# Performance work log

Hardware: AMD Instinct MI355X
Metric: run time of the kernel (lower is better)

## Reference

```python
import jax, jax.numpy as jnp
import numpy as np

N, E, R = 10000, 320000, 32
IN, H, OUT, REL_IN = 256, 256, 256, 768
GAMMA = 10.0


def _seg_softmax(logits, seg, n):
    # numerically stable softmax over edges grouped by target node
    m = jax.ops.segment_max(logits, seg, num_segments=n)
    e = jnp.exp(logits - m[seg])
    s = jax.ops.segment_sum(e, seg, num_segments=n)
    return e / (s[seg] + 1e-16)


def _rgat_layer(x, src, dst, etype, W, q, k, n):
    # per-relation linear transform of all nodes: [N, R, H]
    xt = jnp.einsum('ni,rio->nro', x, W)
    xj = xt[src, etype]          # [E, H] transformed source feats
    xi = xt[dst, etype]          # [E, H] transformed target feats
    logits = jax.nn.leaky_relu((xi * q[etype]).sum(-1) + (xj * k[etype]).sum(-1), 0.2)
    a = _seg_softmax(logits, dst, n)            # [E]
    return jax.ops.segment_sum(a[:, None] * xj, dst, num_segments=n)  # [N, H]


def setup_inputs() -> dict:
    key = jax.random.key(0)
    ks = jax.random.split(key, 16)
    s = 0.05
    return {
        'x': jax.random.normal(ks[0], (N, IN), jnp.float32),
        'edge_index': jax.random.randint(ks[1], (2, E), 0, N, jnp.int32),
        'edge_type': jax.random.randint(ks[2], (E,), 0, R, jnp.int32),
        'W1': jax.random.normal(ks[3], (R, IN, H), jnp.float32) * s,
        'q1': jax.random.normal(ks[4], (R, H), jnp.float32) * s,
        'k1': jax.random.normal(ks[5], (R, H), jnp.float32) * s,
        'W2': jax.random.normal(ks[6], (R, H, H), jnp.float32) * s,
        'q2': jax.random.normal(ks[7], (R, H), jnp.float32) * s,
        'k2': jax.random.normal(ks[8], (R, H), jnp.float32) * s,
        'lin_w': jax.random.normal(ks[9], (H, OUT), jnp.float32) * s,
        'lin_b': jnp.zeros((OUT,), jnp.float32),
        'rel_bert': jax.random.normal(ks[10], (R, REL_IN), jnp.float32),
        'rel_lin_w': jax.random.normal(ks[11], (REL_IN, H), jnp.float32) * s,
        'rel_lin_b': jnp.zeros((H,), jnp.float32),
    }


def reference(x, edge_index, edge_type, W1, q1, k1, W2, q2, k2,
              lin_w, lin_b, rel_bert, rel_lin_w, rel_lin_b):
    src, dst = edge_index[0], edge_index[1]
    h = jax.nn.relu(_rgat_layer(x, src, dst, edge_type, W1, q1, k1, N))
    h = jax.nn.relu(_rgat_layer(h, src, dst, edge_type, W2, q2, k2, N))
    h = h @ lin_w + lin_b                                   # [N, OUT]
    # relation embeddings (dropout omitted: eval-mode determinism)
    rel = jax.nn.relu(rel_bert @ rel_lin_w + rel_lin_b)     # [R, H]
    # TransE scoring per edge
    diff = h[src] + rel[edge_type] - h[dst]                 # [E, OUT]
    score = GAMMA - jnp.abs(diff).sum(-1)                   # [E]
    return score
```

## Files before the change

### kernel.cpp

```cpp
#include <hip/hip_runtime.h>
#include <hip/hip_bf16.h>
#include <stdint.h>

#define R_ 32
#define H_ 256
#define GAMMA_ 10.0f

typedef __attribute__((ext_vector_type(4))) float f32x4;
typedef __attribute__((ext_vector_type(8))) short bf16x8;

__device__ __forceinline__ unsigned short f2b(float f){
  union { float f; unsigned u; } v; v.f = f;
  unsigned r = v.u + 0x7FFFu + ((v.u >> 16) & 1u);
  return (unsigned short)(r >> 16);
}
__device__ __forceinline__ float b2f(unsigned short h){
  union { unsigned u; float f; } v; v.u = ((unsigned)h) << 16; return v.f;
}

__global__ __launch_bounds__(256) void prep_kernel(
    const float* __restrict__ x, unsigned short* __restrict__ xb, int n4,
    const float* __restrict__ W1, unsigned short* __restrict__ Wt1,
    const float* __restrict__ W2, unsigned short* __restrict__ Wt2,
    const float* __restrict__ lin_w, unsigned short* __restrict__ linT,
    const float* __restrict__ q1, const float* __restrict__ k1, float* __restrict__ wqkT1,
    const float* __restrict__ q2, const float* __restrict__ k2, float* __restrict__ wqkT2,
    const float* __restrict__ rb, const float* __restrict__ rw,
    const float* __restrict__ rbias, unsigned short* __restrict__ relb,
    const int* __restrict__ dst, const int* __restrict__ et, int* __restrict__ cnt2, int E,
    int nb0, int nb_tw, int nb_lin, int nb_wqk, int nb_rel, int nb_hist){
  __shared__ float tile[32][33];
  const int bx = blockIdx.x, t = threadIdx.x;
  const int b0 = nb0, b1 = b0 + nb_tw, b2 = b1 + nb_tw, b3 = b2 + nb_lin;
  const int b4 = b3 + nb_wqk, b5 = b4 + nb_wqk, b6 = b5 + nb_rel;

  if (bx < b0){
    int i = bx * 256 + t;
    if (i < n4){
      float4 v = ((const float4*)x)[i];
      ushort4 o; o.x=f2b(v.x); o.y=f2b(v.y); o.z=f2b(v.z); o.w=f2b(v.w);
      ((ushort4*)xb)[i] = o;
    }
    return;
  }
  if (bx < b3){
    const float* W; unsigned short* Wt; int local;
    if (bx < b1){ W = W1; Wt = Wt1; local = bx - b0; }
    else if (bx < b2){ W = W2; Wt = Wt2; local = bx - b1; }
    else { W = lin_w; Wt = linT; local = bx - b2; }
    int i0 = (local & 7) * 32, o0 = ((local >> 3) & 7) * 32, r = local >> 6;
    int tx = t & 31, ty = t >> 5;
    const float* Wr = W + (size_t)r * 65536;
    for (int rr = ty; rr < 32; rr += 8)
      tile[rr][tx] = Wr[(size_t)(i0 + rr) * 256 + o0 + tx];
    __syncthreads();
    unsigned short* outr = Wt + (size_t)r * 65536;
    for (int rr = ty; rr < 32; rr += 8)
      outr[(size_t)(o0 + rr) * 256 + i0 + tx] = f2b(tile[tx][rr]);
    return;
  }
  if (bx < b5){
    bool first = bx < b4;
    int local = bx - (first ? b3 : b4);
    int w = t >> 6, lane = t & 63;
    int p = local * 4 + w;
    int i = p & 255, r = p >> 8;
    const float* W  = first ? W1 : W2;
    const float* qv = first ? q1 : q2;
    const float* kv = first ? k1 : k2;
    const float* row = W + ((size_t)r * 256 + i) * 256;
    float sq = 0.f, sk = 0.f;
    #pragma unroll
    for (int q4 = 0; q4 < 4; ++q4){
      int o = lane + q4 * 64;
      float wv = row[o];
      sq += wv * qv[r * 256 + o];
      sk += wv * kv[r * 256 + o];
    }
    #pragma unroll
    for (int o = 32; o; o >>= 1){ sq += __shfl_xor(sq, o); sk += __shfl_xor(sk, o); }
    if (!lane){
      float* wq = first ? wqkT1 : wqkT2;
      wq[i * 64 + r] = sq; wq[i * 64 + 32 + r] = sk;
    }
    return;
  }
  if (bx < b6){
    int r = bx - b5, h = t;
    float acc = rbias[h];
    const float* br = rb + (size_t)r * 768;
    for (int i = 0; i < 768; ++i) acc += br[i] * rw[(size_t)i * 256 + h];
    relb[r * 256 + h] = f2b(fmaxf(acc, 0.f));
    return;
  }
  {
    int e = (bx - b6) * 256 + t;
    if (e < E){
      int d = dst[e];
      atomicAdd(&cnt2[(d >> 5) * 1024 + (d & 31) * 32 + et[e]], 1);
    }
  }
}

__global__ void totred_kernel(const int* __restrict__ cnt2, int* __restrict__ tot){
  __shared__ int red[256];
  int blk = blockIdx.x, t = threadIdx.x;
  int s = 0;
  #pragma unroll
  for (int q = 0; q < 4; ++q) s += cnt2[blk * 1024 + q * 256 + t];
  red[t] = s; __syncthreads();
  for (int o = 128; o; o >>= 1){ if (t < o) red[t] += red[t + o]; __syncthreads(); }
  if (!t) tot[blk] = red[0];
}
__global__ void scan_kernel(const int* __restrict__ deg, int* __restrict__ off, int n){
  __shared__ int carry;
  __shared__ int buf[1024];
  if (threadIdx.x == 0) carry = 0;
  __syncthreads();
  for (int base = 0; base < n; base += 1024){
    int i = base + threadIdx.x;
    int v = (i < n) ? deg[i] : 0;
    buf[threadIdx.x] = v; __syncthreads();
    for (int o = 1; o < 1024; o <<= 1){
      int t = (threadIdx.x >= o) ? buf[threadIdx.x - o] : 0;
      __syncthreads();
      buf[threadIdx.x] += t;
      __syncthreads();
    }
    if (i < n) off[i] = carry + buf[threadIdx.x] - v;
    __syncthreads();
    if (threadIdx.x == 1023) carry += buf[1023];
    __syncthreads();
  }
  if (threadIdx.x == 0) off[n] = carry;
}
__global__ __launch_bounds__(256) void ps2scan_kernel(const int* __restrict__ cnt2, const int* __restrict__ base,
                                                      int* __restrict__ ps2, int nblk, int nbins){
  __shared__ int sb[1024];
  int blk = blockIdx.x, t = threadIdx.x;
  int orig[4];
  #pragma unroll
  for (int q = 0; q < 4; ++q){ int i = q * 256 + t; orig[q] = cnt2[blk * 1024 + i]; sb[i] = orig[q]; }
  __syncthreads();
  for (int o = 1; o < 1024; o <<= 1){
    int v[4];
    #pragma unroll
    for (int q = 0; q < 4; ++q){ int i = q * 256 + t; v[q] = (i >= o) ? sb[i - o] : 0; }
    __syncthreads();
    #pragma unroll
    for (int q = 0; q < 4; ++q){ int i = q * 256 + t; sb[i] += v[q]; }
    __syncthreads();
  }
  int b = base[blk];
  #pragma unroll
  for (int q = 0; q < 4; ++q){ int i = q * 256 + t; ps2[blk * 1024 + i] = b + sb[i] - orig[q]; }
  if (blk == 0 && t == 0) ps2[nbins] = base[nblk];
}
__global__ void scatter2_kernel(const int* __restrict__ src, const int* __restrict__ dst,
                                const int* __restrict__ et, const int* __restrict__ ps2,
                                int* __restrict__ cur2, int* __restrict__ es_src,
                                int* __restrict__ es_et, int E){
  int e = blockIdx.x * 256 + threadIdx.x;
  if (e >= E) return;
  int d = dst[e], r = et[e];
  int key = (d >> 5) * 1024 + (d & 31) * 32 + r;
  int pos = ps2[key] + atomicAdd(&cur2[key], 1);
  es_src[pos] = src[e];
  es_et[pos]  = r;
}

template<int MODE>
__global__ __launch_bounds__(256) void gemmq_kernel(
    const unsigned short* __restrict__ A, const unsigned short* __restrict__ Bt,
    unsigned short* __restrict__ C, const float* __restrict__ bias, int M, int g_gemm,
    const float* __restrict__ wqkT, float* __restrict__ qdot, float* __restrict__ kdot){
  __shared__ unsigned short As[2][128 * 32];
  __shared__ unsigned short Bs[2][128 * 32];
  const int tid = threadIdx.x, lane = tid & 63, wid = tid >> 6;
  const int bx = blockIdx.x;

  if (MODE == 0 && bx >= g_gemm){
    int node = (bx - g_gemm) * 4 + wid;
    if (node >= M) return;
    float* xr = ((float*)As) + wid * 256;
    ushort4 v = ((const ushort4*)(A + (size_t)node * 256))[lane];
    xr[lane * 4 + 0] = b2f(v.x);
    xr[lane * 4 + 1] = b2f(v.y);
    xr[lane * 4 + 2] = b2f(v.z);
    xr[lane * 4 + 3] = b2f(v.w);
    float acc = 0.f;
    #pragma unroll 8
    for (int kk = 0; kk < 256; ++kk)
      acc = fmaf(xr[kk], wqkT[kk * 64 + lane], acc);
    if (lane < 32) qdot[node * 32 + lane] = acc;
    else           kdot[node * 32 + lane - 32] = acc;
    return;
  }

  const int x = (MODE == 0) ? (bx & 63) : (bx & 1);
  const int y = (MODE == 0) ? (bx >> 6) : (bx >> 1);
  const int r = (MODE == 0) ? (x >> 1) : 0;
  const int nbase = (x & 1) * 128;
  const int mbase = y * 128;
  const int wm = (wid >> 1) * 64, wn = (wid & 1) * 64;
  const int lg = lane >> 4, lr = lane & 15;
  const unsigned short* Brel = Bt + (size_t)r * 65536;

  f32x4 acc[4][4];
  #pragma unroll
  for (int i = 0; i < 4; ++i)
    #pragma unroll
    for (int j = 0; j < 4; ++j) acc[i][j] = (f32x4)0.0f;

  auto stage = [&](int buf, int kt){
    #pragma unroll
    for (int q = 0; q < 2; ++q){
      int ci = q * 256 + tid;
      int row = ci >> 2, p = ci & 3;
      int gch = p ^ ((row >> 1) & 3);
      int grow = mbase + row; if (grow >= M) grow = M - 1;
      const unsigned short* ga = A + (size_t)grow * 256 + kt * 32 + gch * 8;
      __builtin_amdgcn_global_load_lds((const __attribute__((address_space(1))) void*)ga,
          (__attribute__((address_space(3))) void*)(As[buf] + (size_t)ci * 8), 16, 0, 0);
      const unsigned short* gb = Brel + (size_t)(nbase + row) * 256 + kt * 32 + gch * 8;
      __builtin_amdgcn_global_load_lds((const __attribute__((address_space(1))) void*)gb,
          (__attribute__((address_space(3))) void*)(Bs[buf] + (size_t)ci * 8), 16, 0, 0);
    }
  };

  stage(0, 0);
  __syncthreads();

  for (int kt = 0; kt < 8; ++kt){
    const int cur = kt & 1;
    if (kt < 7) stage(cur ^ 1, kt + 1);
    bf16x8 af[4], bg[4];
    #pragma unroll
    for (int mi = 0; mi < 4; ++mi){
      int row = wm + mi * 16 + lr;
      int sl = lg ^ ((row >> 1) & 3);
      af[mi] = *(const bf16x8*)&As[cur][row * 32 + sl * 8];
    }
    #pragma unroll
    for (int ni = 0; ni < 4; ++ni){
      int row = wn + ni * 16 + lr;
      int sl = lg ^ ((row >> 1) & 3);
      bg[ni] = *(const bf16x8*)&Bs[cur][row * 32 + sl * 8];
    }
    #pragma unroll
    for (int mi = 0; mi < 4; ++mi)
      #pragma unroll
      for (int ni = 0; ni < 4; ++ni)
        acc[mi][ni] = __builtin_amdgcn_mfma_f32_16x16x32_bf16(af[mi], bg[ni], acc[mi][ni], 0, 0, 0);
    __syncthreads();
  }

  #pragma unroll
  for (int mi = 0; mi < 4; ++mi){
    #pragma unroll
    for (int j = 0; j < 4; ++j){
      int rowm = mbase + wm + mi * 16 + lg * 4 + j;
      if (rowm >= M) continue;
      #pragma unroll
      for (int ni = 0; ni < 4; ++ni){
        int col = nbase + wn + ni * 16 + lr;
        float v = acc[mi][ni][j];
        if (MODE == 0) C[((size_t)r * M + rowm) * H_ + col] = f2b(v);
        else           C[(size_t)rowm * H_ + col] = f2b(v + bias[col]);
      }
    }
  }
}

__global__ void attn_agg_kernel(const unsigned short* __restrict__ xt, const float* __restrict__ qdot,
                                const float* __restrict__ kdot, const int* __restrict__ ps2,
                                const int* __restrict__ es_src, const int* __restrict__ es_et,
                                float* __restrict__ a, unsigned short* __restrict__ hout, int n){
  int w = threadIdx.x >> 6, lane = threadIdx.x & 63;
  int node = blockIdx.x * 4 + w;
  if (node >= n) return;
  int kb = (node >> 5) * 1024 + (node & 31) * 32;
  int s = 0, e = 0;
  float qd = 0.f;
  if (lane < 32){
    s = ps2[kb + lane]; e = ps2[kb + lane + 1];
    qd = qdot[node * 32 + lane];
  }
  float m = -1e30f;
  for (int j = s; j < e; ++j){
    float z = qd + kdot[es_src[j] * 32 + lane];
    z = (z > 0.f) ? z : 0.2f * z;
    a[j] = z;
    m = fmaxf(m, z);
  }
  #pragma unroll
  for (int o = 32; o; o >>= 1) m = fmaxf(m, __shfl_xor(m, o));
  float sum = 0.f;
  for (int j = s; j < e; ++j){
    float ez = __expf(a[j] - m);
    a[j] = ez; sum += ez;
  }
  #pragma unroll
  for (int o = 32; o; o >>= 1) sum += __shfl_xor(sum, o);
  float inv = 1.0f / (sum + 1e-16f);
  int s0 = ps2[kb], s1 = ps2[kb + 32];
  float a0 = 0.f, a1 = 0.f, a2 = 0.f, a3 = 0.f;
  int j = s0;
  for (; j + 4 <= s1; j += 4){
    int sc0 = es_src[j],   et0 = es_et[j];
    int sc1 = es_src[j+1], et1 = es_et[j+1];
    int sc2 = es_src[j+2], et2 = es_et[j+2];
    int sc3 = es_src[j+3], et3 = es_et[j+3];
    float w0 = a[j], w1 = a[j+1], w2 = a[j+2], w3 = a[j+3];
    ushort4 v0 = ((const ushort4*)(xt + ((size_t)et0 * n + sc0) * 256))[lane];
    ushort4 v1 = ((const ushort4*)(xt + ((size_t)et1 * n + sc1) * 256))[lane];
    ushort4 v2 = ((const ushort4*)(xt + ((size_t)et2 * n + sc2) * 256))[lane];
    ushort4 v3 = ((const ushort4*)(xt + ((size_t)et3 * n + sc3) * 256))[lane];
    a0 += w0*b2f(v0.x) + w1*b2f(v1.x) + w2*b2f(v2.x) + w3*b2f(v3.x);
    a1 += w0*b2f(v0.y) + w1*b2f(v1.y) + w2*b2f(v2.y) + w3*b2f(v3.y);
    a2 += w0*b2f(v0.z) + w1*b2f(v1.z) + w2*b2f(v2.z) + w3*b2f(v3.z);
    a3 += w0*b2f(v0.w) + w1*b2f(v1.w) + w2*b2f(v2.w) + w3*b2f(v3.w);
  }
  for (; j < s1; ++j){
    int sc = es_src[j], et = es_et[j];
    float wv = a[j];
    ushort4 v = ((const ushort4*)(xt + ((size_t)et * n + sc) * 256))[lane];
    a0 = fmaf(wv, b2f(v.x), a0);
    a1 = fmaf(wv, b2f(v.y), a1);
    a2 = fmaf(wv, b2f(v.z), a2);
    a3 = fmaf(wv, b2f(v.w), a3);
  }
  ushort4 o;
  o.x = f2b(fmaxf(a0 * inv, 0.f)); o.y = f2b(fmaxf(a1 * inv, 0.f));
  o.z = f2b(fmaxf(a2 * inv, 0.f)); o.w = f2b(fmaxf(a3 * inv, 0.f));
  ((ushort4*)(hout + (size_t)node * H_))[lane] = o;
}

__global__ void score_kernel(const unsigned short* __restrict__ hb, const unsigned short* __restrict__ relb,
                             const int* __restrict__ src_a, const int* __restrict__ dst_a,
                             const int* __restrict__ et_a, float* __restrict__ out, int E){
  int e = blockIdx.x * 4 + (threadIdx.x >> 6);
  int lane = threadIdx.x & 63;
  if (e >= E) return;
  int s = src_a[e], d = dst_a[e], r = et_a[e];
  ushort4 a4 = ((const ushort4*)(hb + (size_t)s * H_))[lane];
  ushort4 b4 = ((const ushort4*)(hb + (size_t)d * H_))[lane];
  ushort4 r4 = ((const ushort4*)(relb + (size_t)r * H_))[lane];
  float sum = fabsf(b2f(a4.x) + b2f(r4.x) - b2f(b4.x))
            + fabsf(b2f(a4.y) + b2f(r4.y) - b2f(b4.y))
            + fabsf(b2f(a4.z) + b2f(r4.z) - b2f(b4.z))
            + fabsf(b2f(a4.w) + b2f(r4.w) - b2f(b4.w));
  #pragma unroll
  for (int o = 32; o; o >>= 1) sum += __shfl_xor(sum, o);
  if (!lane) out[e] = GAMMA_ - sum;
}

extern "C" void kernel_launch(void* const* d_in, const int* in_sizes, int n_in,
                              void* d_out, int out_size, void* d_ws, size_t ws_size,
                              hipStream_t stream){
  const float* x         = (const float*)d_in[0];
  const int*   edge_idx  = (const int*)d_in[1];
  const int*   edge_type = (const int*)d_in[2];
  const float* W1        = (const float*)d_in[3];
  const float* q1        = (const float*)d_in[4];
  const float* k1        = (const float*)d_in[5];
  const float* W2        = (const float*)d_in[6];
  const float* q2        = (const float*)d_in[7];
  const float* k2        = (const float*)d_in[8];
  const float* lin_w     = (const float*)d_in[9];
  const float* lin_b     = (const float*)d_in[10];
  const float* rel_bert  = (const float*)d_in[11];
  const float* rel_lin_w = (const float*)d_in[12];
  const float* rel_lin_b = (const float*)d_in[13];
  float* score = (float*)d_out;

  const int Nn = in_sizes[0] / H_;
  const int E  = in_sizes[1] / 2;
  const int* src_a = edge_idx;
  const int* dst_a = edge_idx + E;
  const int NBLK  = (Nn + 31) / 32;
  const int NBINS = NBLK * 1024;

  char* ws = (char*)d_ws;
  size_t cur_off = 0;
  auto carve = [&](size_t bytes)->char*{
    char* p = ws + cur_off;
    cur_off += (bytes + 255) & ~(size_t)255;
    return p;
  };
  unsigned short* xt   = (unsigned short*)carve((size_t)Nn * R_ * H_ * 2);
  unsigned short* xb   = (unsigned short*)carve((size_t)Nn * H_ * 2);
  unsigned short* h1   = (unsigned short*)carve((size_t)Nn * H_ * 2);
  unsigned short* h2   = (unsigned short*)carve((size_t)Nn * H_ * 2);
  unsigned short* outb = (unsigned short*)carve((size_t)Nn * H_ * 2);
  unsigned short* Wt1  = (unsigned short*)carve((size_t)R_ * 65536 * 2);
  unsigned short* Wt2  = (unsigned short*)carve((size_t)R_ * 65536 * 2);
  unsigned short* linT = (unsigned short*)carve(65536 * 2);
  unsigned short* relb = (unsigned short*)carve(R_ * H_ * 2);
  float* wqkT1 = (float*)carve(64 * H_ * 4);
  float* wqkT2 = (float*)carve(64 * H_ * 4);
  float* qdot  = (float*)carve((size_t)Nn * R_ * 4);
  float* kdot  = (float*)carve((size_t)Nn * R_ * 4);
  int* cnt2    = (int*)carve((size_t)NBINS * 4);
  int* cur2    = (int*)carve((size_t)NBINS * 4);
  int* tot     = (int*)carve((size_t)NBLK * 4);
  int* baseA   = (int*)carve((size_t)(NBLK + 1) * 4);
  int* ps2     = (int*)carve((size_t)(NBINS + 1) * 4);
  int* es_src  = (int*)carve((size_t)E * 4);
  int* es_et   = (int*)carve((size_t)E * 4);
  float* attn  = (float*)carve((size_t)E * 4);
  (void)ws_size; (void)n_in; (void)out_size;

  const int mt = (Nn + 127) / 128;
  const int g_gemm = 64 * mt;
  const int nqd = (Nn + 3) / 4;

  const int n4 = Nn * H_ / 4;
  const int nb0 = (n4 + 255) / 256, nb_tw = 2048, nb_lin = 64, nb_wqk = 2048, nb_rel = 32;
  const int nb_hist = (E + 255) / 256;
  const int nprep = nb0 + 2 * nb_tw + nb_lin + 2 * nb_wqk + nb_rel + nb_hist;

  hipMemsetAsync(cnt2, 0, (size_t)NBINS * 4, stream);
  hipMemsetAsync(cur2, 0, (size_t)NBINS * 4, stream);

  prep_kernel<<<nprep, 256, 0, stream>>>(
      x, xb, n4, W1, Wt1, W2, Wt2, lin_w, linT,
      q1, k1, wqkT1, q2, k2, wqkT2,
      rel_bert, rel_lin_w, rel_lin_b, relb,
      dst_a, edge_type, cnt2, E,
      nb0, nb_tw, nb_lin, nb_wqk, nb_rel, nb_hist);

  totred_kernel<<<NBLK, 256, 0, stream>>>(cnt2, tot);
  scan_kernel<<<1, 1024, 0, stream>>>(tot, baseA, NBLK);
  ps2scan_kernel<<<NBLK, 256, 0, stream>>>(cnt2, baseA, ps2, NBLK, NBINS);
  scatter2_kernel<<<(E + 255) / 256, 256, 0, stream>>>(src_a, dst_a, edge_type, ps2, cur2, es_src, es_et, E);

  gemmq_kernel<0><<<g_gemm + nqd, 256, 0, stream>>>(xb, Wt1, xt, nullptr, Nn, g_gemm, wqkT1, qdot, kdot);
  attn_agg_kernel<<<nqd, 256, 0, stream>>>(xt, qdot, kdot, ps2, es_src, es_et, attn, h1, Nn);

  gemmq_kernel<0><<<g_gemm + nqd, 256, 0, stream>>>(h1, Wt2, xt, nullptr, Nn, g_gemm, wqkT2, qdot, kdot);
  attn_agg_kernel<<<nqd, 256, 0, stream>>>(xt, qdot, kdot, ps2, es_src, es_et, attn, h2, Nn);

  gemmq_kernel<1><<<2 * mt, 256, 0, stream>>>(h2, linT, outb, lin_b, Nn, 2 * mt, nullptr, nullptr, nullptr);
  score_kernel<<<(E + 3) / 4, 256, 0, stream>>>(outb, relb, src_a, dst_a, edge_type, score, E);
}
```

Measured before the change: 402.4 us.

## Double K-tile depth in bf16 GEMM and stage epilogue through LDS for vector stores

The GEMM now uses a K tile of 64 instead of 32, with a new 8-chunk XOR swizzle, which halves the number of main-loop iterations and barriers. The output tile is first written to padded LDS and then stored to global memory as 16-byte vectors instead of scattered 2-byte stores. The cost is doubled LDS use per block, which can lower occupancy, plus an extra barrier and an LDS round trip in the epilogue.

```diff
diff --git a/kernel.cpp b/kernel.cpp
--- a/kernel.cpp
+++ b/kernel.cpp
@@ -174,8 +174,8 @@
     const unsigned short* __restrict__ A, const unsigned short* __restrict__ Bt,
     unsigned short* __restrict__ C, const float* __restrict__ bias, int M, int g_gemm,
     const float* __restrict__ wqkT, float* __restrict__ qdot, float* __restrict__ kdot){
-  __shared__ unsigned short As[2][128 * 32];
-  __shared__ unsigned short Bs[2][128 * 32];
+  __shared__ unsigned short As[2][128 * 64];
+  __shared__ unsigned short Bs[2][128 * 64];
   const int tid = threadIdx.x, lane = tid & 63, wid = tid >> 6;
   const int bx = blockIdx.x;
 
@@ -214,60 +214,75 @@
 
   auto stage = [&](int buf, int kt){
     #pragma unroll
-    for (int q = 0; q < 2; ++q){
-      int ci = q * 256 + tid;
-      int row = ci >> 2, p = ci & 3;
-      int gch = p ^ ((row >> 1) & 3);
+    for (int q = 0; q < 4; ++q){
+      int ci  = (q * 4 + wid) * 64 + lane;
+      int row = ci >> 3, p = ci & 7;
+      int gch = p ^ (row & 7);
       int grow = mbase + row; if (grow >= M) grow = M - 1;
-      const unsigned short* ga = A + (size_t)grow * 256 + kt * 32 + gch * 8;
+      const unsigned short* ga = A + (size_t)grow * 256 + kt * 64 + gch * 8;
       __builtin_amdgcn_global_load_lds((const __attribute__((address_space(1))) void*)ga,
-          (__attribute__((address_space(3))) void*)(As[buf] + (size_t)ci * 8), 16, 0, 0);
-      const unsigned short* gb = Brel + (size_t)(nbase + row) * 256 + kt * 32 + gch * 8;
+          (__attribute__((address_space(3))) void*)(As[buf] + (size_t)(q * 4 + wid) * 512), 16, 0, 0);
+      const unsigned short* gb = Brel + (size_t)(nbase + row) * 256 + kt * 64 + gch * 8;
       __builtin_amdgcn_global_load_lds((const __attribute__((address_space(1))) void*)gb,
-          (__attribute__((address_space(3))) void*)(Bs[buf] + (size_t)ci * 8), 16, 0, 0);
+          (__attribute__((address_space(3))) void*)(Bs[buf] + (size_t)(q * 4 + wid) * 512), 16, 0, 0);
     }
   };
 
   stage(0, 0);
   __syncthreads();
 
-  for (int kt = 0; kt < 8; ++kt){
+  for (int kt = 0; kt < 4; ++kt){
     const int cur = kt & 1;
-    if (kt < 7) stage(cur ^ 1, kt + 1);
-    bf16x8 af[4], bg[4];
-    #pragma unroll
-    for (int mi = 0; mi < 4; ++mi){
-      int row = wm + mi * 16 + lr;
-      int sl = lg ^ ((row >> 1) & 3);
-      af[mi] = *(const bf16x8*)&As[cur][row * 32 + sl * 8];
-    }
-    #pragma unroll
-    for (int ni = 0; ni < 4; ++ni){
-      int row = wn + ni * 16 + lr;
-      int sl = lg ^ ((row >> 1) & 3);
-      bg[ni] = *(const bf16x8*)&Bs[cur][row * 32 + sl * 8];
-    }
-    #pragma unroll
-    for (int mi = 0; mi < 4; ++mi)
+    if (kt < 3) stage(cur ^ 1, kt + 1);
+    #pragma unroll
+    for (int kk = 0; kk < 2; ++kk){
+      bf16x8 af[4], bg[4];
       #pragma unroll
-      for (int ni = 0; ni < 4; ++ni)
-        acc[mi][ni] = __builtin_amdgcn_mfma_f32_16x16x32_bf16(af[mi], bg[ni], acc[mi][ni], 0, 0, 0);
-    __syncthreads();
-  }
-
-  #pragma unroll
-  for (int mi = 0; mi < 4; ++mi){
-    #pragma unroll
-    for (int j = 0; j < 4; ++j){
-      int rowm = mbase + wm + mi * 16 + lg * 4 + j;
-      if (rowm >= M) continue;
+      for (int mi = 0; mi < 4; ++mi){
+        int row = wm + mi * 16 + lr;
+        int pc = (lg + kk * 4) ^ (row & 7);
+        af[mi] = *(const bf16x8*)&As[cur][row * 64 + pc * 8];
+      }
       #pragma unroll
       for (int ni = 0; ni < 4; ++ni){
-        int col = nbase + wn + ni * 16 + lr;
+        int row = wn + ni * 16 + lr;
+        int pc = (lg + kk * 4) ^ (row & 7);
+        bg[ni] = *(const bf16x8*)&Bs[cur][row * 64 + pc * 8];
+      }
+      #pragma unroll
+      for (int mi = 0; mi < 4; ++mi)
+        #pragma unroll
+        for (int ni = 0; ni < 4; ++ni)
+          acc[mi][ni] = __builtin_amdgcn_mfma_f32_16x16x32_bf16(af[mi], bg[ni], acc[mi][ni], 0, 0, 0);
+    }
+    __syncthreads();
+  }
+
+  unsigned short* c_lds = (unsigned short*)As;
+  #pragma unroll
+  for (int mi = 0; mi < 4; ++mi){
+    #pragma unroll
+    for (int j = 0; j < 4; ++j){
+      int row = wm + mi * 16 + lg * 4 + j;
+      #pragma unroll
+      for (int ni = 0; ni < 4; ++ni){
+        int col = wn + ni * 16 + lr;
         float v = acc[mi][ni][j];
-        if (MODE == 0) C[((size_t)r * M + rowm) * H_ + col] = f2b(v);
-        else           C[(size_t)rowm * H_ + col] = f2b(v + bias[col]);
+        if (MODE == 1) v += bias[nbase + col];
+        c_lds[row * 136 + col] = f2b(v);
       }
+    }
+  }
+  __syncthreads();
+  #pragma unroll
+  for (int it = 0; it < 8; ++it){
+    int c = it * 256 + tid;
+    int row = c >> 4, ch = c & 15;
+    int rowm = mbase + row;
+    if (rowm < M){
+      bf16x8 v = *(const bf16x8*)&c_lds[row * 136 + ch * 8];
+      if (MODE == 0) *(bf16x8*)&C[((size_t)r * M + rowm) * H_ + nbase + ch * 8] = v;
+      else           *(bf16x8*)&C[(size_t)rowm * H_ + nbase + ch * 8] = v;
     }
   }
 }
```

New measurement: 397.8 us. About the same (-1.1%).
